# Optimization experiments

Measured on AMD Instinct MI355X. Metric: run time of the kernel, lower is better.

## Reference

```python
import jax, jax.numpy as jnp
import numpy as np

N, E, R, D, P = 40000, 640000, 500, 128, 3

def setup_inputs() -> dict:
    key = jax.random.key(0)
    ks = jax.random.split(key, 14)
    return {
        "h": jax.random.normal(ks[0], (N, D), jnp.float32),
        "pos_enc": jax.random.normal(ks[1], (N, P), jnp.float32),
        "norm": jax.random.uniform(ks[2], (N, 1), jnp.float32),
        "emb_rel": jax.random.normal(ks[3], (R, D), jnp.float32),
        "W_hp": jax.random.normal(ks[4], (D + P, D), jnp.float32) / np.sqrt(D + P),
        "b_hp": jax.random.normal(ks[5], (D,), jnp.float32) * 0.01,
        "weight_neighbor": jax.random.normal(ks[6], (D, D), jnp.float32) / np.sqrt(D),
        "loop_weight": jax.random.normal(ks[7], (D, D), jnp.float32) / np.sqrt(D),
        "evolve_loop_weight": jax.random.normal(ks[8], (D, D), jnp.float32) / np.sqrt(D),
        "loop_weight_p": jax.random.normal(ks[9], (P, P), jnp.float32),
        "evolve_loop_weight_p": jax.random.normal(ks[10], (P, P), jnp.float32),
        "edge_src": jax.random.randint(ks[11], (E,), 0, N),
        "edge_dst": jax.random.randint(ks[12], (E,), 0, N),
        "edge_type": jax.random.randint(ks[13], (E,), 0, R),
    }

def reference(h, pos_enc, norm, emb_rel, W_hp, b_hp, weight_neighbor,
              loop_weight, evolve_loop_weight, loop_weight_p, evolve_loop_weight_p,
              edge_src, edge_dst, edge_type):
    n = h.shape[0]
    # self-loop: nodes with in-degree > 0 use loop_weight, else evolve_loop_weight
    in_deg = jax.ops.segment_sum(jnp.ones_like(edge_dst, dtype=h.dtype), edge_dst, num_segments=n)
    has_in = (in_deg > 0)[:, None]
    loop_msg = jnp.where(has_in, h @ loop_weight, h @ evolve_loop_weight)
    loop_msg_p = jnp.where(has_in, pos_enc @ loop_weight_p, pos_enc @ evolve_loop_weight_p)
    # per-edge message: embedding_hp(cat(h_src, pos_src)) + rel_emb[type], then weight_neighbor
    src_feat = jnp.concatenate([h[edge_src], pos_enc[edge_src]], axis=1)  # [E, D+P]
    e_h = src_feat @ W_hp + b_hp                                          # [E, D]
    msg = (e_h + emb_rel[edge_type]) @ weight_neighbor                    # [E, D]
    # scatter-sum to destination nodes, then norm scaling (apply_func)
    agg = jax.ops.segment_sum(msg, edge_dst, num_segments=n) * norm       # [N, D]
    node_repr = jax.nn.relu(agg + loop_msg)
    pos_out = jax.nn.relu(pos_enc + loop_msg_p)
    return node_repr, pos_out
```

## Files before the change

kernel.cpp:

```cpp
#include <hip/hip_runtime.h>


#define BS 1536
#define CAP2 48
#define CH 8192

typedef __bf16 bf16x8 __attribute__((ext_vector_type(8)));
typedef float f32x4 __attribute__((ext_vector_type(4)));
typedef unsigned short u16x4 __attribute__((ext_vector_type(4)));

__device__ inline unsigned short f2bf(float f) {
    unsigned u = __float_as_uint(f);
    u += 0x7fffu + ((u >> 16) & 1u);
    return (unsigned short)(u >> 16);
}
__device__ inline float bflo(unsigned u) { return __uint_as_float(u << 16); }
__device__ inline float bfhi(unsigned u) { return __uint_as_float(u & 0xffff0000u); }

__global__ __launch_bounds__(256) void k_pack(const float* __restrict__ Whp,
                                              int* __restrict__ gcnt,
                                              unsigned short* __restrict__ Whpfrag,
                                              int nbkt) {
    const int gid = blockIdx.x * blockDim.x + threadIdx.x;
    const int gs = gridDim.x * blockDim.x;
    for (int i = gid; i < nbkt; i += gs) gcnt[i] = 0;
    for (int i = gid; i < 16384; i += gs) {
        int j = i & 7, l = (i >> 3) & 63, nt = (i >> 9) & 7, c = i >> 12;
        int k = c * 32 + ((l >> 4) << 3) + j;
        int n = nt * 16 + (l & 15);
        Whpfrag[i] = f2bf(Whp[k * 128 + n]);
    }
}

__global__ __launch_bounds__(512) void k_comb(const float* __restrict__ h,
                                              const float* __restrict__ pos,
                                              const float* __restrict__ Whp,
                                              const unsigned short* __restrict__ Whpfrag,
                                              unsigned short* __restrict__ t,
                                              unsigned short* __restrict__ h16,
                                              const int* __restrict__ esrc,
                                              const int* __restrict__ edst,
                                              const int* __restrict__ etyp, int E,
                                              int* __restrict__ gcnt,
                                              unsigned* __restrict__ gbuf,
                                              const float* __restrict__ emb, int embN,
                                              const float* __restrict__ Wn,
                                              const float* __restrict__ Lw,
                                              unsigned short* __restrict__ emb16,
                                              unsigned short* __restrict__ Wfrag,
                                              int nBB, int nPB,
                                              int nbkt, int N) {
    __shared__ unsigned short hsh[64][136];
    __shared__ float WpS[3][128];
    __shared__ float posS[64][4];
    const int tid = threadIdx.x;

    if (blockIdx.x < nBB) {
        int* lcnt = reinterpret_cast<int*>(&hsh[0][0]);
        int* lbase = lcnt + 1280;
        const int e0 = blockIdx.x * CH;
        const int eN = min(E - e0, CH);
        for (int i = tid; i < nbkt; i += 512) lcnt[i] = 0;
        __syncthreads();
        for (int base = tid * 4; base < eN; base += 2048) {
            if (base + 3 < eN) {
                int4 d4 = *reinterpret_cast<const int4*>(&edst[e0 + base]);
                atomicAdd(&lcnt[d4.x >> 5], 1);
                atomicAdd(&lcnt[d4.y >> 5], 1);
                atomicAdd(&lcnt[d4.z >> 5], 1);
                atomicAdd(&lcnt[d4.w >> 5], 1);
            } else {
                for (int k = 0; k < 4 && base + k < eN; k++)
                    atomicAdd(&lcnt[edst[e0 + base + k] >> 5], 1);
            }
        }
        __syncthreads();
        for (int i = tid; i < nbkt; i += 512) {
            int c = lcnt[i];
            lbase[i] = c ? atomicAdd(&gcnt[i], c) : 0;
        }
        __syncthreads();
        for (int i = tid; i < nbkt; i += 512) lcnt[i] = 0;
        __syncthreads();
        for (int base = tid * 4; base < eN; base += 2048) {
            if (base + 3 < eN) {
                int4 d4 = *reinterpret_cast<const int4*>(&edst[e0 + base]);
                int4 s4 = *reinterpret_cast<const int4*>(&esrc[e0 + base]);
                int4 t4 = *reinterpret_cast<const int4*>(&etyp[e0 + base]);
                int dd[4] = {d4.x, d4.y, d4.z, d4.w};
                int ss[4] = {s4.x, s4.y, s4.z, s4.w};
                int tt[4] = {t4.x, t4.y, t4.z, t4.w};
#pragma unroll
                for (int k = 0; k < 4; k++) {
                    int b = dd[k] >> 5;
                    unsigned val = (unsigned)(dd[k] & 31) | ((unsigned)ss[k] << 5)
                                 | ((unsigned)tt[k] << 21);
                    int off = atomicAdd(&lcnt[b], 1);
                    gbuf[(size_t)b * BS + min(lbase[b] + off, BS - 1)] = val;
                }
            } else {
                for (int k = 0; k < 4 && base + k < eN; k++) {
                    int d = edst[e0 + base + k];
                    int b = d >> 5;
                    unsigned val = (unsigned)(d & 31) | ((unsigned)esrc[e0 + base + k] << 5)
                                 | ((unsigned)etyp[e0 + base + k] << 21);
                    int off = atomicAdd(&lcnt[b], 1);
                    gbuf[(size_t)b * BS + min(lbase[b] + off, BS - 1)] = val;
                }
            }
        }
        return;
    }

    if (blockIdx.x < nBB + nPB) {
        const int base = (blockIdx.x - nBB) * 512 + tid;
        const int gs = nPB * 512;
        for (int i = base; i < 32768; i += gs) {
            int j = i & 7, l = (i >> 3) & 63, nt = (i >> 9) & 7, c = i >> 12;
            int k = c * 32 + ((l >> 4) << 3) + j;
            int n = nt * 16 + (l & 15);
            float v = (k < 128) ? Wn[k * 128 + n] : Lw[(k - 128) * 128 + n];
            Wfrag[i] = f2bf(v);
        }
        for (int i = base; i < embN; i += gs) emb16[i] = f2bf(emb[i]);
        return;
    }

    const int rbase = (blockIdx.x - nBB - nPB) * 64;
    const int w = tid >> 6, l = tid & 63;
    for (int i = tid; i < 384; i += 512) WpS[i >> 7][i & 127] = Whp[128 * 128 + i];
    if (tid < 192) {
        int r = tid / 3, j = tid % 3;
        int row = rbase + r;
        posS[r][j] = (row < N) ? pos[(size_t)row * 3 + j] : 0.f;
    }
#pragma unroll
    for (int it = 0; it < 4; it++) {
        int qid = tid + it * 512;
        int rr = qid >> 5, cq = qid & 31;
        int row = rbase + rr;
        u16x4 v = {0, 0, 0, 0};
        if (row < N) {
            float4 a = *reinterpret_cast<const float4*>(h + (size_t)row * 128 + cq * 4);
            v[0] = f2bf(a.x); v[1] = f2bf(a.y); v[2] = f2bf(a.z); v[3] = f2bf(a.w);
            *reinterpret_cast<u16x4*>(&h16[(size_t)row * 128 + cq * 4]) = v;
        }
        *reinterpret_cast<u16x4*>(&hsh[rr][cq * 4]) = v;
    }
    __syncthreads();

    f32x4 acc[4];
#pragma unroll
    for (int i = 0; i < 4; i++) acc[i] = (f32x4){0.f, 0.f, 0.f, 0.f};
    const int rt = w >> 1, ch = w & 1;
#pragma unroll
    for (int c = 0; c < 4; c++) {
        bf16x8 a = *reinterpret_cast<const bf16x8*>(&hsh[rt * 16 + (l & 15)][c * 32 + (l >> 4) * 8]);
        const bf16x8* Bp = reinterpret_cast<const bf16x8*>(Whpfrag) + (size_t)c * 512;
#pragma unroll
        for (int n2 = 0; n2 < 4; n2++) {
            bf16x8 b = Bp[(ch * 4 + n2) * 64 + l];
            acc[n2] = __builtin_amdgcn_mfma_f32_16x16x32_bf16(a, b, acc[n2], 0, 0, 0);
        }
    }
    const int lrow0 = rt * 16 + ((l >> 4) << 2);
#pragma unroll
    for (int n2 = 0; n2 < 4; n2++) {
        int col = (ch * 4 + n2) * 16 + (l & 15);
        float w0 = WpS[0][col], w1 = WpS[1][col], w2 = WpS[2][col];
#pragma unroll
        for (int r = 0; r < 4; r++) {
            int lr = lrow0 + r;
            int grow = rbase + lr;
            if (grow < N) {
                float v = acc[n2][r] + posS[lr][0] * w0 + posS[lr][1] * w1 + posS[lr][2] * w2;
                t[(size_t)grow * 128 + col] = f2bf(v);
            }
        }
    }
}

__global__ __launch_bounds__(512) void k_fused(const float* __restrict__ h,
                                               const float* __restrict__ pos,
                                               const float* __restrict__ nrm,
                                               const float* __restrict__ bhp,
                                               const unsigned short* __restrict__ t,
                                               const unsigned short* __restrict__ h16,
                                               const unsigned short* __restrict__ emb16,
                                               const int* __restrict__ gcnt,
                                               const unsigned* __restrict__ gbuf,
                                               const unsigned short* __restrict__ Wfrag,
                                               const float* __restrict__ Ew,
                                               const float* __restrict__ Lwp,
                                               const float* __restrict__ Ewp,
                                               float* __restrict__ out, int N) {
    __shared__ unsigned eplists[32][CAP2];
    __shared__ int lcnt2[32];
    __shared__ unsigned short x0sh[32][136];
    __shared__ unsigned short hsh[32][136];
    __shared__ float bsh[128];
    __shared__ float nrmS[32];
    __shared__ int zrowsS[32];
    __shared__ int nzS;
    const int tid = threadIdx.x;
    const int rbase = blockIdx.x * 32;
    const int w = tid >> 6, lane = tid & 63;
    const int half = lane >> 5;
    const int g = (lane >> 4) & 1, l16 = lane & 15;

    if (tid < 128) bsh[tid] = bhp[tid];
    if (tid == 128) nzS = 0;
    if (tid < 32) {
        int row = rbase + tid;
        nrmS[tid] = (row < N) ? nrm[row] : 0.f;
        lcnt2[tid] = 0;
    }
    __syncthreads();

    const int cntB = min(gcnt[blockIdx.x], BS);
    for (int i = tid; i < cntB; i += 512) {
        unsigned v = gbuf[(size_t)blockIdx.x * BS + i];
        int d = v & 31;
        int off = atomicAdd(&lcnt2[d], 1);
        if (off < CAP2) eplists[d][off] = v >> 5;
    }
    __syncthreads();

    if (tid < 32) {
        int row = rbase + tid;
        if (row < N && lcnt2[tid] == 0) {
            int o = atomicAdd(&nzS, 1);
            zrowsS[o] = tid;
        }
    }

    const uint4* tw4 = reinterpret_cast<const uint4*>(t);
    const uint4* ew4 = reinterpret_cast<const uint4*>(emb16);

#pragma unroll 1
    for (int p = 0; p < 2; p++) {
        const int base2 = p * 16 + w * 2;
        const int vl = base2 + half;
        const int m = min(lcnt2[vl], CAP2);
        const int mm = max(min(lcnt2[base2], CAP2), min(lcnt2[base2 + 1], CAP2));
        float a[8];
#pragma unroll
        for (int r = 0; r < 8; r++) a[r] = 0.f;
        const unsigned* epr = &eplists[vl][0];
#pragma unroll 1
        for (int j = 0; j < mm; j += 8) {
            uint4 tv[4], ev[4];
            float sel[4];
#pragma unroll
            for (int u = 0; u < 4; u++) {
                int idx = j + 2 * u + g;
                unsigned pe = epr[min(idx, CAP2 - 1)];
                bool val = idx < m;
                unsigned pk = val ? pe : 0u;
                sel[u] = val ? 1.f : 0.f;
                tv[u] = tw4[(pk & 0xffffu) * 16u + l16];
                ev[u] = ew4[(pk >> 16) * 16u + l16];
            }
#pragma unroll
            for (int u = 0; u < 4; u++) {
                a[0] = fmaf(sel[u], bflo(tv[u].x) + bflo(ev[u].x), a[0]);
                a[1] = fmaf(sel[u], bfhi(tv[u].x) + bfhi(ev[u].x), a[1]);
                a[2] = fmaf(sel[u], bflo(tv[u].y) + bflo(ev[u].y), a[2]);
                a[3] = fmaf(sel[u], bfhi(tv[u].y) + bfhi(ev[u].y), a[3]);
                a[4] = fmaf(sel[u], bflo(tv[u].z) + bflo(ev[u].z), a[4]);
                a[5] = fmaf(sel[u], bfhi(tv[u].z) + bfhi(ev[u].z), a[5]);
                a[6] = fmaf(sel[u], bflo(tv[u].w) + bflo(ev[u].w), a[6]);
                a[7] = fmaf(sel[u], bfhi(tv[u].w) + bfhi(ev[u].w), a[7]);
            }
        }
#pragma unroll
        for (int r = 0; r < 8; r++) a[r] += __shfl_xor(a[r], 16);
        if (g == 0) {
            float dg = (float)lcnt2[vl], nf = nrmS[vl];
            unsigned pk4[4];
#pragma unroll
            for (int q = 0; q < 4; q++) {
                float lo = nf * (a[2 * q]     + dg * bsh[l16 * 8 + 2 * q]);
                float hi = nf * (a[2 * q + 1] + dg * bsh[l16 * 8 + 2 * q + 1]);
                pk4[q] = (unsigned)f2bf(lo) | ((unsigned)f2bf(hi) << 16);
            }
            *reinterpret_cast<uint4*>(&x0sh[vl][l16 * 8]) =
                make_uint4(pk4[0], pk4[1], pk4[2], pk4[3]);
        }
    }

    {
        int rr = tid >> 4, q = tid & 15;
        int row = rbase + rr;
        uint4 v = make_uint4(0, 0, 0, 0);
        if (row < N)
            v = reinterpret_cast<const uint4*>(h16)[(size_t)row * 16 + q];
        *reinterpret_cast<uint4*>(&hsh[rr][q * 8]) = v;
    }
    __syncthreads();

    f32x4 acc[2];
    acc[0] = (f32x4){0.f, 0.f, 0.f, 0.f};
    acc[1] = (f32x4){0.f, 0.f, 0.f, 0.f};
    const int rt = w >> 2, ch = w & 3;
    const int arow = rt * 16 + (lane & 15);
#pragma unroll
    for (int c = 0; c < 8; c++) {
        uint4 raw;
        if (c < 4)
            raw = *reinterpret_cast<const uint4*>(&x0sh[arow][c * 32 + (lane >> 4) * 8]);
        else
            raw = *reinterpret_cast<const uint4*>(&hsh[arow][(c & 3) * 32 + (lane >> 4) * 8]);
        bf16x8 a = *reinterpret_cast<bf16x8*>(&raw);
        const bf16x8* Bp = reinterpret_cast<const bf16x8*>(Wfrag) + (size_t)c * 512;
#pragma unroll
        for (int n2 = 0; n2 < 2; n2++) {
            bf16x8 b = Bp[(ch * 2 + n2) * 64 + lane];
            acc[n2] = __builtin_amdgcn_mfma_f32_16x16x32_bf16(a, b, acc[n2], 0, 0, 0);
        }
    }
    const int lrow0 = rt * 16 + ((lane >> 4) << 2);
#pragma unroll
    for (int n2 = 0; n2 < 2; n2++) {
        int col = (ch * 2 + n2) * 16 + (lane & 15);
#pragma unroll
        for (int r = 0; r < 4; r++) {
            int lr = lrow0 + r;
            int grow = rbase + lr;
            if (grow < N && lcnt2[lr] > 0)
                out[(size_t)grow * 128 + col] = fmaxf(acc[n2][r], 0.f);
        }
    }
    for (int zi = 0; zi < nzS; zi++) {
        int r = zrowsS[zi];
        int row = rbase + r;
        if (tid < 128) {
            float accp = 0.f;
            for (int k = 0; k < 128; k++)
                accp += h[(size_t)row * 128 + k] * Ew[k * 128 + tid];
            out[(size_t)row * 128 + tid] = fmaxf(accp, 0.f);
        }
    }
    if (tid < 32) {
        int row = rbase + tid;
        if (row < N) {
            float p0 = pos[(size_t)row * 3 + 0];
            float p1 = pos[(size_t)row * 3 + 1];
            float p2 = pos[(size_t)row * 3 + 2];
            const float* M = (lcnt2[tid] > 0) ? Lwp : Ewp;
            float o0 = p0 + (p0 * M[0] + p1 * M[3] + p2 * M[6]);
            float o1 = p1 + (p0 * M[1] + p1 * M[4] + p2 * M[7]);
            float o2 = p2 + (p0 * M[2] + p1 * M[5] + p2 * M[8]);
            size_t base = (size_t)N * 128 + (size_t)row * 3;
            out[base + 0] = fmaxf(o0, 0.f);
            out[base + 1] = fmaxf(o1, 0.f);
            out[base + 2] = fmaxf(o2, 0.f);
        }
    }
}

extern "C" void kernel_launch(void* const* d_in, const int* in_sizes, int n_in,
                              void* d_out, int out_size, void* d_ws, size_t ws_size,
                              hipStream_t stream) {
    const float* h   = (const float*)d_in[0];
    const float* pos = (const float*)d_in[1];
    const float* nrm = (const float*)d_in[2];
    const float* emb = (const float*)d_in[3];
    const float* Whp = (const float*)d_in[4];
    const float* bhp = (const float*)d_in[5];
    const float* Wn  = (const float*)d_in[6];
    const float* Lw  = (const float*)d_in[7];
    const float* Ew  = (const float*)d_in[8];
    const float* Lwp = (const float*)d_in[9];
    const float* Ewp = (const float*)d_in[10];
    const int* esrc  = (const int*)d_in[11];
    const int* edst  = (const int*)d_in[12];
    const int* etyp  = (const int*)d_in[13];

    const int N = in_sizes[2];
    const int E = in_sizes[11];
    const int embN = in_sizes[3];

    float* out = (float*)d_out;

    char* wsb = (char*)d_ws;
    size_t off = 0;
    auto nalloc = [&](size_t bytes) { char* p = wsb + off; off += (bytes + 255) & ~(size_t)255; return p; };
    const int nbkt = (N + 31) / 32;
    unsigned short* t       = (unsigned short*)nalloc((size_t)N * 128 * 2);
    unsigned short* h16     = (unsigned short*)nalloc((size_t)N * 128 * 2);
    int*            gcnt    = (int*)nalloc((size_t)nbkt * 4);
    unsigned*       gbuf    = (unsigned*)nalloc((size_t)nbkt * BS * 4);
    unsigned short* emb16   = (unsigned short*)nalloc((size_t)embN * 2);
    unsigned short* Wfrag   = (unsigned short*)nalloc(32768 * 2);
    unsigned short* Whpfrag = (unsigned short*)nalloc(16384 * 2);

    k_pack<<<64, 256, 0, stream>>>(Whp, gcnt, Whpfrag, nbkt);
    const int nTB = (N + 63) / 64;
    const int nBB = (E + CH - 1) / CH;
    const int nPB = 32;
    k_comb<<<nBB + nPB + nTB, 512, 0, stream>>>(h, pos, Whp, Whpfrag, t, h16,
                                                esrc, edst, etyp, E,
                                                gcnt, gbuf,
                                                emb, embN, Wn, Lw,
                                                emb16, Wfrag, nBB, nPB, nbkt, N);
    k_fused<<<nbkt, 512, 0, stream>>>(h, pos, nrm, bhp, t, h16, emb16, gcnt, gbuf,
                                      Wfrag, Ew, Lwp, Ewp, out, N);
}
```

Baseline: 64.95 us.

## Fold W_hp and emb_rel into weight_neighbor, aggregate raw h before GEMM

Uses linearity to precompute W_hp·Wn, pos-rows·Wn and (emb+b)·Wn. The per-node t = h·W_hp GEMM and its intermediate buffer go away. The fused kernel now gathers bf16 h rows and the precomputed relation rows separately and sums source positions with LDS atomics. It then applies a single GEMM on the aggregated h. The precompute uses naive per-thread dot products (R×128×128 plus 16K×128) inside k_comb, and the edge-binning chunk size is halved with more prep blocks.

```diff
diff --git a/kernel.cpp b/kernel.cpp
--- a/kernel.cpp
+++ b/kernel.cpp
@@ -3,7 +3,7 @@
 
 #define BS 1536
 #define CAP2 48
-#define CH 8192
+#define CH 4096
 
 typedef __bf16 bf16x8 __attribute__((ext_vector_type(8)));
 typedef float f32x4 __attribute__((ext_vector_type(4)));
@@ -17,47 +17,29 @@
 __device__ inline float bflo(unsigned u) { return __uint_as_float(u << 16); }
 __device__ inline float bfhi(unsigned u) { return __uint_as_float(u & 0xffff0000u); }
 
-__global__ __launch_bounds__(256) void k_pack(const float* __restrict__ Whp,
-                                              int* __restrict__ gcnt,
-                                              unsigned short* __restrict__ Whpfrag,
-                                              int nbkt) {
-    const int gid = blockIdx.x * blockDim.x + threadIdx.x;
-    const int gs = gridDim.x * blockDim.x;
-    for (int i = gid; i < nbkt; i += gs) gcnt[i] = 0;
-    for (int i = gid; i < 16384; i += gs) {
-        int j = i & 7, l = (i >> 3) & 63, nt = (i >> 9) & 7, c = i >> 12;
-        int k = c * 32 + ((l >> 4) << 3) + j;
-        int n = nt * 16 + (l & 15);
-        Whpfrag[i] = f2bf(Whp[k * 128 + n]);
-    }
-}
-
 __global__ __launch_bounds__(512) void k_comb(const float* __restrict__ h,
-                                              const float* __restrict__ pos,
                                               const float* __restrict__ Whp,
-                                              const unsigned short* __restrict__ Whpfrag,
-                                              unsigned short* __restrict__ t,
-                                              unsigned short* __restrict__ h16,
+                                              const float* __restrict__ bhp,
+                                              const float* __restrict__ Wn,
+                                              const float* __restrict__ Lw,
+                                              const float* __restrict__ emb, int R,
                                               const int* __restrict__ esrc,
                                               const int* __restrict__ edst,
                                               const int* __restrict__ etyp, int E,
                                               int* __restrict__ gcnt,
                                               unsigned* __restrict__ gbuf,
-                                              const float* __restrict__ emb, int embN,
-                                              const float* __restrict__ Wn,
-                                              const float* __restrict__ Lw,
-                                              unsigned short* __restrict__ emb16,
-                                              unsigned short* __restrict__ Wfrag,
-                                              int nBB, int nPB,
-                                              int nbkt, int N) {
-    __shared__ unsigned short hsh[64][136];
-    __shared__ float WpS[3][128];
-    __shared__ float posS[64][4];
+                                              unsigned short* __restrict__ h16,
+                                              unsigned short* __restrict__ EWn16,
+                                              unsigned short* __restrict__ WhpWnFrag,
+                                              float* __restrict__ WpW,
+                                              unsigned short* __restrict__ LwFrag,
+                                              int nBB, int nPB, int nbkt, int N) {
+    __shared__ int binLds[2560];
     const int tid = threadIdx.x;
 
     if (blockIdx.x < nBB) {
-        int* lcnt = reinterpret_cast<int*>(&hsh[0][0]);
-        int* lbase = lcnt + 1280;
+        int* lcnt = binLds;
+        int* lbase = binLds + 1280;
         const int e0 = blockIdx.x * CH;
         const int eN = min(E - e0, CH);
         for (int i = tid; i < nbkt; i += 512) lcnt[i] = 0;
@@ -112,93 +94,67 @@
         return;
     }
 
-    if (blockIdx.x < nBB + nPB) {
-        const int base = (blockIdx.x - nBB) * 512 + tid;
-        const int gs = nPB * 512;
-        for (int i = base; i < 32768; i += gs) {
-            int j = i & 7, l = (i >> 3) & 63, nt = (i >> 9) & 7, c = i >> 12;
-            int k = c * 32 + ((l >> 4) << 3) + j;
-            int n = nt * 16 + (l & 15);
-            float v = (k < 128) ? Wn[k * 128 + n] : Lw[(k - 128) * 128 + n];
-            Wfrag[i] = f2bf(v);
-        }
-        for (int i = base; i < embN; i += gs) emb16[i] = f2bf(emb[i]);
-        return;
-    }
-
-    const int rbase = (blockIdx.x - nBB - nPB) * 64;
-    const int w = tid >> 6, l = tid & 63;
-    for (int i = tid; i < 384; i += 512) WpS[i >> 7][i & 127] = Whp[128 * 128 + i];
-    if (tid < 192) {
-        int r = tid / 3, j = tid % 3;
-        int row = rbase + r;
-        posS[r][j] = (row < N) ? pos[(size_t)row * 3 + j] : 0.f;
-    }
-#pragma unroll
-    for (int it = 0; it < 4; it++) {
-        int qid = tid + it * 512;
-        int rr = qid >> 5, cq = qid & 31;
-        int row = rbase + rr;
-        u16x4 v = {0, 0, 0, 0};
-        if (row < N) {
-            float4 a = *reinterpret_cast<const float4*>(h + (size_t)row * 128 + cq * 4);
-            v[0] = f2bf(a.x); v[1] = f2bf(a.y); v[2] = f2bf(a.z); v[3] = f2bf(a.w);
-            *reinterpret_cast<u16x4*>(&h16[(size_t)row * 128 + cq * 4]) = v;
-        }
-        *reinterpret_cast<u16x4*>(&hsh[rr][cq * 4]) = v;
-    }
-    __syncthreads();
-
-    f32x4 acc[4];
-#pragma unroll
-    for (int i = 0; i < 4; i++) acc[i] = (f32x4){0.f, 0.f, 0.f, 0.f};
-    const int rt = w >> 1, ch = w & 1;
-#pragma unroll
-    for (int c = 0; c < 4; c++) {
-        bf16x8 a = *reinterpret_cast<const bf16x8*>(&hsh[rt * 16 + (l & 15)][c * 32 + (l >> 4) * 8]);
-        const bf16x8* Bp = reinterpret_cast<const bf16x8*>(Whpfrag) + (size_t)c * 512;
-#pragma unroll
-        for (int n2 = 0; n2 < 4; n2++) {
-            bf16x8 b = Bp[(ch * 4 + n2) * 64 + l];
-            acc[n2] = __builtin_amdgcn_mfma_f32_16x16x32_bf16(a, b, acc[n2], 0, 0, 0);
-        }
-    }
-    const int lrow0 = rt * 16 + ((l >> 4) << 2);
-#pragma unroll
-    for (int n2 = 0; n2 < 4; n2++) {
-        int col = (ch * 4 + n2) * 16 + (l & 15);
-        float w0 = WpS[0][col], w1 = WpS[1][col], w2 = WpS[2][col];
-#pragma unroll
-        for (int r = 0; r < 4; r++) {
-            int lr = lrow0 + r;
-            int grow = rbase + lr;
-            if (grow < N) {
-                float v = acc[n2][r] + posS[lr][0] * w0 + posS[lr][1] * w1 + posS[lr][2] * w2;
-                t[(size_t)grow * 128 + col] = f2bf(v);
-            }
-        }
+    const int gid0 = (blockIdx.x - nBB) * 512 + tid;
+    const int gs = nPB * 512;
+    for (int i = gid0; i < N * 32; i += gs) {
+        int row = i >> 5, q = i & 31;
+        float4 a = *reinterpret_cast<const float4*>(h + (size_t)row * 128 + q * 4);
+        u16x4 v;
+        v[0] = f2bf(a.x); v[1] = f2bf(a.y); v[2] = f2bf(a.z); v[3] = f2bf(a.w);
+        *reinterpret_cast<u16x4*>(&h16[(size_t)row * 128 + q * 4]) = v;
+    }
+    for (int i = gid0; i < 16384; i += gs) {
+        int j = i & 7, l = (i >> 3) & 63, nt = (i >> 9) & 7, c = i >> 12;
+        int k = c * 32 + ((l >> 4) << 3) + j;
+        int n = nt * 16 + (l & 15);
+        float s = 0.f;
+#pragma unroll 4
+        for (int q = 0; q < 128; q++) s += Whp[k * 128 + q] * Wn[q * 128 + n];
+        WhpWnFrag[i] = f2bf(s);
+    }
+    for (int i = gid0; i < 384; i += gs) {
+        int r = i >> 7, cc = i & 127;
+        float s = 0.f;
+#pragma unroll 4
+        for (int q = 0; q < 128; q++) s += Whp[(128 + r) * 128 + q] * Wn[q * 128 + cc];
+        WpW[i] = s;
+    }
+    for (int i = gid0; i < R * 128; i += gs) {
+        int t = i >> 7, cc = i & 127;
+        float s = 0.f;
+#pragma unroll 4
+        for (int q = 0; q < 128; q++) s += (emb[t * 128 + q] + bhp[q]) * Wn[q * 128 + cc];
+        EWn16[i] = f2bf(s);
+    }
+    for (int i = gid0; i < 16384; i += gs) {
+        int j = i & 7, l = (i >> 3) & 63, nt = (i >> 9) & 7, c = i >> 12;
+        int k = c * 32 + ((l >> 4) << 3) + j;
+        int n = nt * 16 + (l & 15);
+        LwFrag[i] = f2bf(Lw[k * 128 + n]);
     }
 }
 
 __global__ __launch_bounds__(512) void k_fused(const float* __restrict__ h,
                                                const float* __restrict__ pos,
                                                const float* __restrict__ nrm,
-                                               const float* __restrict__ bhp,
-                                               const unsigned short* __restrict__ t,
                                                const unsigned short* __restrict__ h16,
-                                               const unsigned short* __restrict__ emb16,
+                                               const unsigned short* __restrict__ EWn16,
                                                const int* __restrict__ gcnt,
                                                const unsigned* __restrict__ gbuf,
-                                               const unsigned short* __restrict__ Wfrag,
+                                               const unsigned short* __restrict__ WhpWnFrag,
+                                               const unsigned short* __restrict__ LwFrag,
+                                               const float* __restrict__ WpW,
                                                const float* __restrict__ Ew,
                                                const float* __restrict__ Lwp,
                                                const float* __restrict__ Ewp,
                                                float* __restrict__ out, int N) {
     __shared__ unsigned eplists[32][CAP2];
     __shared__ int lcnt2[32];
-    __shared__ unsigned short x0sh[32][136];
+    __shared__ float psumS[32][4];
+    __shared__ unsigned short hpsumS[32][136];
+    __shared__ unsigned short esumS[32][136];
     __shared__ unsigned short hsh[32][136];
-    __shared__ float bsh[128];
+    __shared__ float WpWS[3][128];
     __shared__ float nrmS[32];
     __shared__ int zrowsS[32];
     __shared__ int nzS;
@@ -208,12 +164,13 @@
     const int half = lane >> 5;
     const int g = (lane >> 4) & 1, l16 = lane & 15;
 
-    if (tid < 128) bsh[tid] = bhp[tid];
-    if (tid == 128) nzS = 0;
+    if (tid < 384) WpWS[tid >> 7][tid & 127] = WpW[tid];
+    if (tid == 448) nzS = 0;
     if (tid < 32) {
         int row = rbase + tid;
         nrmS[tid] = (row < N) ? nrm[row] : 0.f;
         lcnt2[tid] = 0;
+        psumS[tid][0] = 0.f; psumS[tid][1] = 0.f; psumS[tid][2] = 0.f;
     }
     __syncthreads();
 
@@ -223,6 +180,11 @@
         int d = v & 31;
         int off = atomicAdd(&lcnt2[d], 1);
         if (off < CAP2) eplists[d][off] = v >> 5;
+        unsigned src = (v >> 5) & 0xffffu;
+        const float* pp = pos + (size_t)src * 3;
+        atomicAdd(&psumS[d][0], pp[0]);
+        atomicAdd(&psumS[d][1], pp[1]);
+        atomicAdd(&psumS[d][2], pp[2]);
     }
     __syncthreads();
 
@@ -234,8 +196,8 @@
         }
     }
 
-    const uint4* tw4 = reinterpret_cast<const uint4*>(t);
-    const uint4* ew4 = reinterpret_cast<const uint4*>(emb16);
+    const uint4* h4 = reinterpret_cast<const uint4*>(h16);
+    const uint4* e4 = reinterpret_cast<const uint4*>(EWn16);
 
 #pragma unroll 1
     for (int p = 0; p < 2; p++) {
@@ -247,46 +209,39 @@
 #pragma unroll
         for (int r = 0; r < 8; r++) a[r] = 0.f;
         const unsigned* epr = &eplists[vl][0];
+        const uint4* basep = g ? e4 : h4;
 #pragma unroll 1
         for (int j = 0; j < mm; j += 8) {
-            uint4 tv[4], ev[4];
-            float sel[4];
-#pragma unroll
-            for (int u = 0; u < 4; u++) {
-                int idx = j + 2 * u + g;
+            uint4 rv[8];
+#pragma unroll
+            for (int u = 0; u < 8; u++) {
+                int idx = j + u;
                 unsigned pe = epr[min(idx, CAP2 - 1)];
-                bool val = idx < m;
-                unsigned pk = val ? pe : 0u;
-                sel[u] = val ? 1.f : 0.f;
-                tv[u] = tw4[(pk & 0xffffu) * 16u + l16];
-                ev[u] = ew4[(pk >> 16) * 16u + l16];
-            }
-#pragma unroll
-            for (int u = 0; u < 4; u++) {
-                a[0] = fmaf(sel[u], bflo(tv[u].x) + bflo(ev[u].x), a[0]);
-                a[1] = fmaf(sel[u], bfhi(tv[u].x) + bfhi(ev[u].x), a[1]);
-                a[2] = fmaf(sel[u], bflo(tv[u].y) + bflo(ev[u].y), a[2]);
-                a[3] = fmaf(sel[u], bfhi(tv[u].y) + bfhi(ev[u].y), a[3]);
-                a[4] = fmaf(sel[u], bflo(tv[u].z) + bflo(ev[u].z), a[4]);
-                a[5] = fmaf(sel[u], bfhi(tv[u].z) + bfhi(ev[u].z), a[5]);
-                a[6] = fmaf(sel[u], bflo(tv[u].w) + bflo(ev[u].w), a[6]);
-                a[7] = fmaf(sel[u], bfhi(tv[u].w) + bfhi(ev[u].w), a[7]);
-            }
-        }
-#pragma unroll
-        for (int r = 0; r < 8; r++) a[r] += __shfl_xor(a[r], 16);
-        if (g == 0) {
-            float dg = (float)lcnt2[vl], nf = nrmS[vl];
-            unsigned pk4[4];
-#pragma unroll
-            for (int q = 0; q < 4; q++) {
-                float lo = nf * (a[2 * q]     + dg * bsh[l16 * 8 + 2 * q]);
-                float hi = nf * (a[2 * q + 1] + dg * bsh[l16 * 8 + 2 * q + 1]);
-                pk4[q] = (unsigned)f2bf(lo) | ((unsigned)f2bf(hi) << 16);
-            }
-            *reinterpret_cast<uint4*>(&x0sh[vl][l16 * 8]) =
-                make_uint4(pk4[0], pk4[1], pk4[2], pk4[3]);
-        }
+                unsigned pk = (idx < m) ? pe : 0u;
+                unsigned ridx = g ? (pk >> 16) : (pk & 0xffffu);
+                rv[u] = basep[(size_t)ridx * 16u + l16];
+            }
+#pragma unroll
+            for (int u = 0; u < 8; u++) {
+                float s = (j + u < m) ? 1.f : 0.f;
+                a[0] = fmaf(s, bflo(rv[u].x), a[0]);
+                a[1] = fmaf(s, bfhi(rv[u].x), a[1]);
+                a[2] = fmaf(s, bflo(rv[u].y), a[2]);
+                a[3] = fmaf(s, bfhi(rv[u].y), a[3]);
+                a[4] = fmaf(s, bflo(rv[u].z), a[4]);
+                a[5] = fmaf(s, bfhi(rv[u].z), a[5]);
+                a[6] = fmaf(s, bflo(rv[u].w), a[6]);
+                a[7] = fmaf(s, bfhi(rv[u].w), a[7]);
+            }
+        }
+        float nf = nrmS[vl];
+        unsigned pk4[4];
+#pragma unroll
+        for (int q = 0; q < 4; q++) {
+            pk4[q] = (unsigned)f2bf(nf * a[2 * q]) | ((unsigned)f2bf(nf * a[2 * q + 1]) << 16);
+        }
+        unsigned short* dst = g ? &esumS[vl][0] : &hpsumS[vl][0];
+        *reinterpret_cast<uint4*>(&dst[l16 * 8]) = make_uint4(pk4[0], pk4[1], pk4[2], pk4[3]);
     }
 
     {
@@ -307,12 +262,15 @@
 #pragma unroll
     for (int c = 0; c < 8; c++) {
         uint4 raw;
-        if (c < 4)
-            raw = *reinterpret_cast<const uint4*>(&x0sh[arow][c * 32 + (lane >> 4) * 8]);
-        else
+        const bf16x8* Bp;
+        if (c < 4) {
+            raw = *reinterpret_cast<const uint4*>(&hpsumS[arow][c * 32 + (lane >> 4) * 8]);
+            Bp = reinterpret_cast<const bf16x8*>(WhpWnFrag) + (size_t)c * 512;
+        } else {
             raw = *reinterpret_cast<const uint4*>(&hsh[arow][(c & 3) * 32 + (lane >> 4) * 8]);
+            Bp = reinterpret_cast<const bf16x8*>(LwFrag) + (size_t)(c & 3) * 512;
+        }
         bf16x8 a = *reinterpret_cast<bf16x8*>(&raw);
-        const bf16x8* Bp = reinterpret_cast<const bf16x8*>(Wfrag) + (size_t)c * 512;
 #pragma unroll
         for (int n2 = 0; n2 < 2; n2++) {
             bf16x8 b = Bp[(ch * 2 + n2) * 64 + lane];
@@ -323,12 +281,18 @@
 #pragma unroll
     for (int n2 = 0; n2 < 2; n2++) {
         int col = (ch * 2 + n2) * 16 + (lane & 15);
+        float wp0 = WpWS[0][col], wp1 = WpWS[1][col], wp2 = WpWS[2][col];
 #pragma unroll
         for (int r = 0; r < 4; r++) {
             int lr = lrow0 + r;
             int grow = rbase + lr;
-            if (grow < N && lcnt2[lr] > 0)
-                out[(size_t)grow * 128 + col] = fmaxf(acc[n2][r], 0.f);
+            if (grow < N && lcnt2[lr] > 0) {
+                float nfr = nrmS[lr];
+                float es = bflo((unsigned)esumS[lr][col]);
+                float pterm = psumS[lr][0] * wp0 + psumS[lr][1] * wp1 + psumS[lr][2] * wp2;
+                float v = acc[n2][r] + es + nfr * pterm;
+                out[(size_t)grow * 128 + col] = fmaxf(v, 0.f);
+            }
         }
     }
     for (int zi = 0; zi < nzS; zi++) {
@@ -379,7 +343,7 @@
 
     const int N = in_sizes[2];
     const int E = in_sizes[11];
-    const int embN = in_sizes[3];
+    const int R = in_sizes[3] / 128;
 
     float* out = (float*)d_out;
 
@@ -387,23 +351,23 @@
     size_t off = 0;
     auto nalloc = [&](size_t bytes) { char* p = wsb + off; off += (bytes + 255) & ~(size_t)255; return p; };
     const int nbkt = (N + 31) / 32;
-    unsigned short* t       = (unsigned short*)nalloc((size_t)N * 128 * 2);
-    unsigned short* h16     = (unsigned short*)nalloc((size_t)N * 128 * 2);
-    int*            gcnt    = (int*)nalloc((size_t)nbkt * 4);
-    unsigned*       gbuf    = (unsigned*)nalloc((size_t)nbkt * BS * 4);
-    unsigned short* emb16   = (unsigned short*)nalloc((size_t)embN * 2);
-    unsigned short* Wfrag   = (unsigned short*)nalloc(32768 * 2);
-    unsigned short* Whpfrag = (unsigned short*)nalloc(16384 * 2);
-
-    k_pack<<<64, 256, 0, stream>>>(Whp, gcnt, Whpfrag, nbkt);
-    const int nTB = (N + 63) / 64;
+    unsigned short* h16       = (unsigned short*)nalloc((size_t)N * 128 * 2);
+    int*            gcnt      = (int*)nalloc((size_t)nbkt * 4);
+    unsigned*       gbuf      = (unsigned*)nalloc((size_t)nbkt * BS * 4);
+    unsigned short* EWn16     = (unsigned short*)nalloc((size_t)R * 128 * 2);
+    unsigned short* WhpWnFrag = (unsigned short*)nalloc(16384 * 2);
+    unsigned short* LwFrag    = (unsigned short*)nalloc(16384 * 2);
+    float*          WpW       = (float*)nalloc(384 * 4);
+
+    hipMemsetAsync(gcnt, 0, (size_t)nbkt * 4, stream);
+
     const int nBB = (E + CH - 1) / CH;
-    const int nPB = 32;
-    k_comb<<<nBB + nPB + nTB, 512, 0, stream>>>(h, pos, Whp, Whpfrag, t, h16,
-                                                esrc, edst, etyp, E,
-                                                gcnt, gbuf,
-                                                emb, embN, Wn, Lw,
-                                                emb16, Wfrag, nBB, nPB, nbkt, N);
-    k_fused<<<nbkt, 512, 0, stream>>>(h, pos, nrm, bhp, t, h16, emb16, gcnt, gbuf,
-                                      Wfrag, Ew, Lwp, Ewp, out, N);
+    const int nPB = 64;
+    k_comb<<<nBB + nPB, 512, 0, stream>>>(h, Whp, bhp, Wn, Lw, emb, R,
+                                          esrc, edst, etyp, E,
+                                          gcnt, gbuf, h16, EWn16,
+                                          WhpWnFrag, WpW, LwFrag,
+                                          nBB, nPB, nbkt, N);
+    k_fused<<<nbkt, 512, 0, stream>>>(h, pos, nrm, h16, EWn16, gcnt, gbuf,
+                                      WhpWnFrag, LwFrag, WpW, Ew, Lwp, Ewp, out, N);
 }
```

After: 99.28 us. 52.9% more time.
